# Performance work log

Hardware: AMD Instinct MI355X
Metric: run time of the kernel (lower is better)

## Reference

```python
import jax, jax.numpy as jnp
import numpy as np

N_NODES = 100000
N_EDGES = 1600000
D = 128  # conv_channels = [128, 128, 128] -> two GCNConv layers


def setup_inputs() -> dict:
    key = jax.random.key(0)
    ks = jax.random.split(key, 6)
    x = jax.random.normal(ks[0], (N_NODES, D), dtype=jnp.float32)
    edge_index = jax.random.randint(ks[1], (2, N_EDGES), 0, N_NODES, dtype=jnp.int32)
    s = 1.0 / np.sqrt(D)
    W1 = jax.random.uniform(ks[2], (D, D), jnp.float32, -s, s)
    b1 = jnp.zeros((D,), jnp.float32)
    W2 = jax.random.uniform(ks[3], (D, D), jnp.float32, -s, s)
    b2 = jnp.zeros((D,), jnp.float32)
    return {"x": x, "edge_index": edge_index, "W1": W1, "b1": b1, "W2": W2, "b2": b2}


def _gcn_layer(x, W, b, src, dst, norm, n_nodes):
    h = x @ W                       # [N, out]
    msg = h[src] * norm[:, None]    # gather + scale, [E', out]
    agg = jax.ops.segment_sum(msg, dst, num_segments=n_nodes)
    return agg + b


def reference(x, edge_index, W1, b1, W2, b2):
    n = x.shape[0]
    # add_self_loops: append (i, i) for every node
    loop = jnp.arange(n, dtype=edge_index.dtype)
    src = jnp.concatenate([edge_index[0], loop])
    dst = jnp.concatenate([edge_index[1], loop])
    # symmetric GCN normalization: deg over target nodes (unit edge weights)
    deg = jax.ops.segment_sum(jnp.ones_like(src, dtype=x.dtype), dst, num_segments=n)
    dis = jnp.where(deg > 0, jax.lax.rsqrt(deg), 0.0)
    norm = dis[src] * dis[dst]      # [E']

    h = _gcn_layer(x, W1, b1, src, dst, norm, n)
    h = jax.nn.elu(h)
    # dropout p=0.3 is identity in eval mode
    h = _gcn_layer(h, W2, b2, src, dst, norm, n)
    h = jax.nn.elu(h)
    return h
```

## Files before the change

### kernel.cpp

```cpp
#include <hip/hip_runtime.h>
#include <math.h>

#define NN 100000
#define NE 1600000
#define NT (NE + NN)
#define DD 128
#define NB 500
#define BR 200
#define BCAP 4096
#define NCH 2048
#define NBK 782
#define NBG 1563
#define PW 68
#define BMAGIC 21474837u

typedef unsigned int uint;
typedef unsigned short ushort;
typedef __attribute__((ext_vector_type(8))) short bf16x8;
typedef __attribute__((ext_vector_type(4))) float f32x4;

__device__ __forceinline__ uint bfr(float f){
  uint u = __float_as_uint(f);
  return (u + 0x7FFFu + ((u >> 16) & 1u)) >> 16;
}
__device__ __forceinline__ uint pk2(float a, float b){
  return (bfr(a) & 0xFFFFu) | (bfr(b) << 16);
}
__device__ __forceinline__ bf16x8 asbf(uint4 u){
  union { uint4 u; bf16x8 b; } c; c.u = u; return c.b;
}

__global__ __launch_bounds__(256) void k_pre1(const float* __restrict__ W1f, const float* __restrict__ W2f,
    uint* __restrict__ Wt1, uint* __restrict__ Wt2,
    const int* __restrict__ ei, int* __restrict__ gcnt, uint* __restrict__ bedge){
  __shared__ uint   ent[NCH];
  __shared__ ushort bbs[NCH];
  __shared__ int    hist[NB];
  __shared__ int    fl[NB];
  __shared__ int    gb[NB];
  int t = threadIdx.x;
  if (blockIdx.x < 2){
    const float* W = blockIdx.x ? W2f : W1f;
    uint* Wt = blockIdx.x ? Wt2 : Wt1;
    int n = t >> 1, k0 = (t & 1) * 64;
    for (int kk = 0; kk < 64; kk += 2){
      float v0 = W[(size_t)(k0+kk  )*DD + n];
      float v1 = W[(size_t)(k0+kk+1)*DD + n];
      Wt[(size_t)n*64 + ((k0+kk)>>1)] = pk2(v0, v1);
    }
    return;
  }
  int bid = blockIdx.x - 2;
  int base = bid * NCH;
  int nv = NE - base; if (nv > NCH) nv = NCH;
  for (int b = t; b < NB; b += 256){ hist[b] = 0; fl[b] = 0; }
  __syncthreads();
  for (int j = t; j < nv; j += 256){
    int i = base + j;
    uint s = (uint)ei[i];
    uint d = (uint)ei[NE + i];
    uint b = __umulhi(d, BMAGIC);
    uint dl = d - b*BR;
    ent[j] = s | (dl << 17);
    bbs[j] = (ushort)b;
    atomicAdd(&hist[b], 1);
  }
  __syncthreads();
  for (int b = t; b < NB; b += 256){
    int h = hist[b];
    gb[b] = h ? atomicAdd(&gcnt[b*16], h) : 0;
  }
  __syncthreads();
  for (int j = t; j < nv; j += 256){
    uint b = bbs[j];
    int q = atomicAdd(&fl[b], 1);
    bedge[(size_t)b*BCAP + gb[b] + q] = ent[j];
  }
}

__global__ __launch_bounds__(256) void k_pre2(const int* __restrict__ gcnt, int* __restrict__ bbase,
    const uint* __restrict__ bedge, int* __restrict__ deg, float* __restrict__ dis){
  __shared__ int sm[256];
  int t = threadIdx.x;
  if (blockIdx.x == 0){
    int i0 = 2*t, i1 = 2*t + 1;
    int v0 = (i0 < NB) ? (gcnt[i0*16] + BR) : 0;
    int v1 = (i1 < NB) ? (gcnt[i1*16] + BR) : 0;
    int p = v0 + v1;
    sm[t] = p;
    __syncthreads();
    for (int off = 1; off < 256; off <<= 1){
      int a = (t >= off) ? sm[t-off] : 0;
      __syncthreads();
      sm[t] += a;
      __syncthreads();
    }
    int excl = sm[t] - p;
    if (i0 < NB) bbase[i0] = excl;
    if (i1 < NB) bbase[i1] = excl + v0;
    return;
  }
  int b = blockIdx.x - 1;
  int* cl = sm;
  if (t < BR) cl[t] = 0;
  __syncthreads();
  int cnt = gcnt[b*16];
  for (int e = t; e < cnt; e += 256){
    atomicAdd(&cl[bedge[(size_t)b*BCAP + e] >> 17], 1);
  }
  __syncthreads();
  if (t < BR){
    int n = b*BR + t;
    int dg = cl[t];
    deg[n] = dg;
    dis[n] = rsqrtf((float)(dg + 1));
  }
}

template<int IN_BF16>
__device__ __forceinline__ void gemm_body(uint* __restrict__ Ws, uint* __restrict__ Xs,
    const void* __restrict__ Xv, const uint* __restrict__ Wt,
    const float* __restrict__ dis, uint* __restrict__ Y, int row0){
  int t = threadIdx.x;
  #pragma unroll
  for (int it = 0; it < 8; ++it){
    int f = it*256 + t;
    uint4 v = ((const uint4*)Wt)[f];
    int row = f >> 4, c4 = f & 15;
    *(uint4*)&Ws[row*PW + c4*4] = v;
  }
  if (!IN_BF16){
    const float* X = (const float*)Xv;
    #pragma unroll
    for (int it = 0; it < 8; ++it){
      int f = it*256 + t;
      int row = f >> 5, c4 = f & 31;
      int gr = row0 + row;
      float4 v = (gr < NN) ? ((const float4*)X)[(size_t)gr*32 + c4]
                           : make_float4(0.f,0.f,0.f,0.f);
      uint2 p; p.x = pk2(v.x, v.y); p.y = pk2(v.z, v.w);
      *(uint2*)&Xs[row*PW + c4*2] = p;
    }
  } else {
    const uint* X = (const uint*)Xv;
    #pragma unroll
    for (int it = 0; it < 4; ++it){
      int f = it*256 + t;
      int row = f >> 4, c4 = f & 15;
      int gr = row0 + row;
      uint4 v = (gr < NN) ? ((const uint4*)X)[(size_t)gr*16 + c4]
                          : make_uint4(0,0,0,0);
      *(uint4*)&Xs[row*PW + c4*4] = v;
    }
  }
  __syncthreads();

  int wv = t >> 6, l = t & 63;
  int g = l >> 4, li = l & 15;
  int rb = wv*16 + li;
  int r  = row0 + rb;
  f32x4 acc[8];
  #pragma unroll
  for (int i = 0; i < 8; ++i) acc[i] = (f32x4){0.f,0.f,0.f,0.f};

  #pragma unroll
  for (int ks = 0; ks < 4; ++ks){
    int c = (ks*4 + g)*4;
    bf16x8 bfrag = asbf(*(const uint4*)&Xs[rb*PW + c]);
    #pragma unroll
    for (int nt = 0; nt < 8; ++nt){
      bf16x8 afrag = asbf(*(const uint4*)&Ws[(nt*16 + li)*PW + c]);
      acc[nt] = __builtin_amdgcn_mfma_f32_16x16x32_bf16(afrag, bfrag, acc[nt], 0, 0, 0);
    }
  }
  if (r < NN){
    float dr = dis[r];
    #pragma unroll
    for (int nt = 0; nt < 8; ++nt){
      uint2 o;
      o.x = pk2(acc[nt][0]*dr, acc[nt][1]*dr);
      o.y = pk2(acc[nt][2]*dr, acc[nt][3]*dr);
      *(uint2*)&Y[(size_t)r*64 + nt*8 + g*2] = o;
    }
  }
}

__global__ __launch_bounds__(256, 3) void k_bg(const int* __restrict__ gcnt,
    const int* __restrict__ bbase, const uint* __restrict__ bedge,
    const int* __restrict__ deg, const float* __restrict__ dis,
    int* __restrict__ rowptr, uint* __restrict__ es,
    const float* __restrict__ X, const uint* __restrict__ Wt1, uint* __restrict__ H){
  __shared__ uint smem[192*PW];
  int t = threadIdx.x;
  if (blockIdx.x >= NB){
    gemm_body<0>(smem, smem + 128*PW, X, Wt1, dis, H, (blockIdx.x - NB)*64);
    return;
  }
  int b = blockIdx.x;
  int base = bbase[b];
  int* cl = (int*)smem;
  int* fl = cl + BR;
  int* pf = cl + 2*BR;
  if (t < BR){ cl[t] = deg[b*BR + t]; fl[t] = 0; }
  __syncthreads();
  int v = (t < BR) ? (cl[t] + 1) : 0;
  pf[t] = v;
  __syncthreads();
  for (int off = 1; off < 256; off <<= 1){
    int a = (t >= off) ? pf[t-off] : 0;
    __syncthreads();
    pf[t] += a;
    __syncthreads();
  }
  if (t < BR){
    int n  = b*BR + t;
    int p0 = base + pf[t] - v;
    rowptr[n] = p0;
    es[p0 + cl[t]] = (uint)n;
  }
  if (b == NB-1 && t == 0) rowptr[NN] = NT;
  __syncthreads();
  int cnt = gcnt[b*16];
  for (int e = t; e < cnt; e += 256){
    uint u = bedge[(size_t)b*BCAP + e];
    int  dloc = u >> 17;
    int  q  = atomicAdd(&fl[dloc], 1);
    int  p0 = base + pf[dloc] - (cl[dloc] + 1);
    es[p0 + q] = u & 0x1FFFFu;
  }
}

__global__ __launch_bounds__(256, 3) void k_gemm2(const uint* __restrict__ X,
    const uint* __restrict__ Wt, const float* __restrict__ dis, uint* __restrict__ Y){
  __shared__ uint smem[192*PW];
  gemm_body<1>(smem, smem + 128*PW, X, Wt, dis, Y, blockIdx.x*64);
}

template<int OUT_BF16>
__global__ __launch_bounds__(256) void k_agg(const uint* __restrict__ H,
    const int* __restrict__ rowptr, const float* __restrict__ dis,
    const uint* __restrict__ es, const float* __restrict__ bias,
    void* __restrict__ outv){
  int wid  = threadIdx.x >> 6;
  int lane = threadIdx.x & 63;
  int n = blockIdx.x*4 + wid;
  int e0 = rowptr[n];
  int e1 = rowptr[n+1];
  float a0 = 0.f, a1 = 0.f, a2 = 0.f, a3 = 0.f;
  int e = e0;

#define ASTEP(k,A,B) { uint s##k = es[e+k]; \
    uint h##k = H[(size_t)s##k*64 + lane]; \
    A += __uint_as_float(h##k << 16); \
    B += __uint_as_float(h##k & 0xFFFF0000u); }

  for (; e + 16 <= e1; e += 16){
    ASTEP( 0,a0,a1) ASTEP( 1,a2,a3) ASTEP( 2,a0,a1) ASTEP( 3,a2,a3)
    ASTEP( 4,a0,a1) ASTEP( 5,a2,a3) ASTEP( 6,a0,a1) ASTEP( 7,a2,a3)
    ASTEP( 8,a0,a1) ASTEP( 9,a2,a3) ASTEP(10,a0,a1) ASTEP(11,a2,a3)
    ASTEP(12,a0,a1) ASTEP(13,a2,a3) ASTEP(14,a0,a1) ASTEP(15,a2,a3)
  }
  for (; e + 4 <= e1; e += 4){
    ASTEP(0,a0,a1) ASTEP(1,a2,a3) ASTEP(2,a0,a1) ASTEP(3,a2,a3)
  }
  for (; e < e1; ++e){
    ASTEP(0,a0,a1)
  }
#undef ASTEP

  float dn = dis[n];
  float2 b = *(const float2*)&bias[lane*2];
  float v0 = fmaf(dn, a0 + a2, b.x);
  float v1 = fmaf(dn, a1 + a3, b.y);
  v0 = (v0 > 0.f) ? v0 : expm1f(v0);
  v1 = (v1 > 0.f) ? v1 : expm1f(v1);
  if (OUT_BF16){
    ((uint*)outv)[(size_t)n*64 + lane] = pk2(v0, v1);
  } else {
    float2 o; o.x = v0; o.y = v1;
    *(float2*)&((float*)outv)[(size_t)n*DD + lane*2] = o;
  }
}


extern "C" void kernel_launch(void* const* d_in, const int* in_sizes, int n_in,
                              void* d_out, int out_size, void* d_ws, size_t ws_size,
                              hipStream_t stream){
  const float* x  = (const float*)d_in[0];
  const int*   ei = (const int*)d_in[1];
  const float* W1 = (const float*)d_in[2];
  const float* b1 = (const float*)d_in[3];
  const float* W2 = (const float*)d_in[4];
  const float* b2 = (const float*)d_in[5];

  int*   ws_i   = (int*)d_ws;
  int*   gcnt   = ws_i + 0;
  int*   bbase  = ws_i + 8000;
  float* dis    = (float*)(ws_i + 8576);
  int*   rowptr = ws_i + 108608;
  int*   deg    = ws_i + 208704;
  uint*  Wt1    = (uint*)(ws_i + 308736);
  uint*  Wt2    = (uint*)(ws_i + 316928);
  uint*  es     = (uint*)(ws_i + 325120);
  uint*  bedge  = (uint*)(ws_i + 2025152);
  uint*  out1   = (uint*)(ws_i + 2025152);
  uint*  H      = (uint*)(ws_i + 8425152);
  uint*  H2     = H;

  hipMemsetAsync(gcnt, 0, 8000*sizeof(int), stream);

  k_pre1<<<NBK + 2, 256, 0, stream>>>(W1, W2, Wt1, Wt2, ei, gcnt, bedge);
  k_pre2<<<NB + 1,  256, 0, stream>>>(gcnt, bbase, bedge, deg, dis);
  k_bg  <<<NB + NBG,256, 0, stream>>>(gcnt, bbase, bedge, deg, dis, rowptr, es, x, Wt1, H);
  k_agg<1><<<25000, 256, 0, stream>>>(H, rowptr, dis, es, b1, out1);
  k_gemm2 <<<NBG,   256, 0, stream>>>(out1, Wt2, dis, H2);
  k_agg<0><<<25000, 256, 0, stream>>>(H2, rowptr, dis, es, b2, d_out);
}
```

Measured before the change: 233.7 us.

## Pack source-norm weights into edge list and overlap GEMM1 with bucketing

Removes the dis[r] row scaling from the GEMMs. Instead, each CSR edge entry now carries bf16(dis[src]) in its top 15 bits, and the aggregation kernel applies that weight with an FMA. Because GEMM1 no longer depends on the degree, it can run in the same launch as the edge bucketing pass. The hipMemset is replaced by a small init kernel and the CSR build becomes its own kernel. The cost is a bf16-rounded per-edge weight and an extra dis gather during CSR construction; the 15-bit field also relies on dis being positive and below 2.

Measured after the change: 243.8 us. 4.3% more time.

```diff
diff --git a/kernel.cpp b/kernel.cpp
--- a/kernel.cpp
+++ b/kernel.cpp
@@ -30,28 +30,105 @@
   union { uint4 u; bf16x8 b; } c; c.u = u; return c.b;
 }
 
-__global__ __launch_bounds__(256) void k_pre1(const float* __restrict__ W1f, const float* __restrict__ W2f,
-    uint* __restrict__ Wt1, uint* __restrict__ Wt2,
-    const int* __restrict__ ei, int* __restrict__ gcnt, uint* __restrict__ bedge){
-  __shared__ uint   ent[NCH];
-  __shared__ ushort bbs[NCH];
-  __shared__ int    hist[NB];
-  __shared__ int    fl[NB];
-  __shared__ int    gb[NB];
+__global__ __launch_bounds__(256) void k_init(const float* __restrict__ W1f, const float* __restrict__ W2f,
+    uint* __restrict__ Wt1, uint* __restrict__ Wt2, int* __restrict__ gcnt){
   int t = threadIdx.x;
-  if (blockIdx.x < 2){
-    const float* W = blockIdx.x ? W2f : W1f;
-    uint* Wt = blockIdx.x ? Wt2 : Wt1;
-    int n = t >> 1, k0 = (t & 1) * 64;
-    for (int kk = 0; kk < 64; kk += 2){
-      float v0 = W[(size_t)(k0+kk  )*DD + n];
-      float v1 = W[(size_t)(k0+kk+1)*DD + n];
-      Wt[(size_t)n*64 + ((k0+kk)>>1)] = pk2(v0, v1);
-    }
+  if (blockIdx.x == 2){
+    for (int i = t; i < 8000; i += 256) gcnt[i] = 0;
     return;
   }
-  int bid = blockIdx.x - 2;
-  int base = bid * NCH;
+  const float* W = blockIdx.x ? W2f : W1f;
+  uint* Wt = blockIdx.x ? Wt2 : Wt1;
+  int n = t >> 1, k0 = (t & 1) * 64;
+  for (int kk = 0; kk < 64; kk += 2){
+    float v0 = W[(size_t)(k0+kk  )*DD + n];
+    float v1 = W[(size_t)(k0+kk+1)*DD + n];
+    Wt[(size_t)n*64 + ((k0+kk)>>1)] = pk2(v0, v1);
+  }
+}
+
+template<int IN_BF16>
+__device__ __forceinline__ void gemm_body(uint* __restrict__ Ws, uint* __restrict__ Xs,
+    const void* __restrict__ Xv, const uint* __restrict__ Wt,
+    uint* __restrict__ Y, int row0){
+  int t = threadIdx.x;
+  #pragma unroll
+  for (int it = 0; it < 8; ++it){
+    int f = it*256 + t;
+    uint4 v = ((const uint4*)Wt)[f];
+    int row = f >> 4, c4 = f & 15;
+    *(uint4*)&Ws[row*PW + c4*4] = v;
+  }
+  if (!IN_BF16){
+    const float* X = (const float*)Xv;
+    #pragma unroll
+    for (int it = 0; it < 8; ++it){
+      int f = it*256 + t;
+      int row = f >> 5, c4 = f & 31;
+      int gr = row0 + row;
+      float4 v = (gr < NN) ? ((const float4*)X)[(size_t)gr*32 + c4]
+                           : make_float4(0.f,0.f,0.f,0.f);
+      uint2 p; p.x = pk2(v.x, v.y); p.y = pk2(v.z, v.w);
+      *(uint2*)&Xs[row*PW + c4*2] = p;
+    }
+  } else {
+    const uint* X = (const uint*)Xv;
+    #pragma unroll
+    for (int it = 0; it < 4; ++it){
+      int f = it*256 + t;
+      int row = f >> 4, c4 = f & 15;
+      int gr = row0 + row;
+      uint4 v = (gr < NN) ? ((const uint4*)X)[(size_t)gr*16 + c4]
+                          : make_uint4(0,0,0,0);
+      *(uint4*)&Xs[row*PW + c4*4] = v;
+    }
+  }
+  __syncthreads();
+
+  int wv = t >> 6, l = t & 63;
+  int g = l >> 4, li = l & 15;
+  int rb = wv*16 + li;
+  int r  = row0 + rb;
+  f32x4 acc[8];
+  #pragma unroll
+  for (int i = 0; i < 8; ++i) acc[i] = (f32x4){0.f,0.f,0.f,0.f};
+
+  #pragma unroll
+  for (int ks = 0; ks < 4; ++ks){
+    int c = (ks*4 + g)*4;
+    bf16x8 bfrag = asbf(*(const uint4*)&Xs[rb*PW + c]);
+    #pragma unroll
+    for (int nt = 0; nt < 8; ++nt){
+      bf16x8 afrag = asbf(*(const uint4*)&Ws[(nt*16 + li)*PW + c]);
+      acc[nt] = __builtin_amdgcn_mfma_f32_16x16x32_bf16(afrag, bfrag, acc[nt], 0, 0, 0);
+    }
+  }
+  if (r < NN){
+    #pragma unroll
+    for (int nt = 0; nt < 8; ++nt){
+      uint2 o;
+      o.x = pk2(acc[nt][0], acc[nt][1]);
+      o.y = pk2(acc[nt][2], acc[nt][3]);
+      *(uint2*)&Y[(size_t)r*64 + nt*8 + g*2] = o;
+    }
+  }
+}
+
+__global__ __launch_bounds__(256, 3) void k_A(const int* __restrict__ ei,
+    int* __restrict__ gcnt, uint* __restrict__ bedge,
+    const float* __restrict__ X, const uint* __restrict__ Wt1, uint* __restrict__ H){
+  __shared__ uint smem[192*PW];
+  int t = threadIdx.x;
+  if (blockIdx.x >= NBK){
+    gemm_body<0>(smem, smem + 128*PW, X, Wt1, H, (blockIdx.x - NBK)*64);
+    return;
+  }
+  uint*   ent  = smem;
+  ushort* bbs  = (ushort*)(smem + NCH);
+  int*    hist = (int*)(smem + NCH + NCH/2);
+  int*    fl   = hist + NB;
+  int*    gb   = fl + NB;
+  int base = blockIdx.x * NCH;
   int nv = NE - base; if (nv > NCH) nv = NCH;
   for (int b = t; b < NB; b += 256){ hist[b] = 0; fl[b] = 0; }
   __syncthreads();
@@ -78,7 +155,7 @@
   }
 }
 
-__global__ __launch_bounds__(256) void k_pre2(const int* __restrict__ gcnt, int* __restrict__ bbase,
+__global__ __launch_bounds__(256) void k_B(const int* __restrict__ gcnt, int* __restrict__ bbase,
     const uint* __restrict__ bedge, int* __restrict__ deg, float* __restrict__ dis){
   __shared__ int sm[256];
   int t = threadIdx.x;
@@ -117,90 +194,15 @@
   }
 }
 
-template<int IN_BF16>
-__device__ __forceinline__ void gemm_body(uint* __restrict__ Ws, uint* __restrict__ Xs,
-    const void* __restrict__ Xv, const uint* __restrict__ Wt,
-    const float* __restrict__ dis, uint* __restrict__ Y, int row0){
-  int t = threadIdx.x;
-  #pragma unroll
-  for (int it = 0; it < 8; ++it){
-    int f = it*256 + t;
-    uint4 v = ((const uint4*)Wt)[f];
-    int row = f >> 4, c4 = f & 15;
-    *(uint4*)&Ws[row*PW + c4*4] = v;
-  }
-  if (!IN_BF16){
-    const float* X = (const float*)Xv;
-    #pragma unroll
-    for (int it = 0; it < 8; ++it){
-      int f = it*256 + t;
-      int row = f >> 5, c4 = f & 31;
-      int gr = row0 + row;
-      float4 v = (gr < NN) ? ((const float4*)X)[(size_t)gr*32 + c4]
-                           : make_float4(0.f,0.f,0.f,0.f);
-      uint2 p; p.x = pk2(v.x, v.y); p.y = pk2(v.z, v.w);
-      *(uint2*)&Xs[row*PW + c4*2] = p;
-    }
-  } else {
-    const uint* X = (const uint*)Xv;
-    #pragma unroll
-    for (int it = 0; it < 4; ++it){
-      int f = it*256 + t;
-      int row = f >> 4, c4 = f & 15;
-      int gr = row0 + row;
-      uint4 v = (gr < NN) ? ((const uint4*)X)[(size_t)gr*16 + c4]
-                          : make_uint4(0,0,0,0);
-      *(uint4*)&Xs[row*PW + c4*4] = v;
-    }
-  }
-  __syncthreads();
-
-  int wv = t >> 6, l = t & 63;
-  int g = l >> 4, li = l & 15;
-  int rb = wv*16 + li;
-  int r  = row0 + rb;
-  f32x4 acc[8];
-  #pragma unroll
-  for (int i = 0; i < 8; ++i) acc[i] = (f32x4){0.f,0.f,0.f,0.f};
-
-  #pragma unroll
-  for (int ks = 0; ks < 4; ++ks){
-    int c = (ks*4 + g)*4;
-    bf16x8 bfrag = asbf(*(const uint4*)&Xs[rb*PW + c]);
-    #pragma unroll
-    for (int nt = 0; nt < 8; ++nt){
-      bf16x8 afrag = asbf(*(const uint4*)&Ws[(nt*16 + li)*PW + c]);
-      acc[nt] = __builtin_amdgcn_mfma_f32_16x16x32_bf16(afrag, bfrag, acc[nt], 0, 0, 0);
-    }
-  }
-  if (r < NN){
-    float dr = dis[r];
-    #pragma unroll
-    for (int nt = 0; nt < 8; ++nt){
-      uint2 o;
-      o.x = pk2(acc[nt][0]*dr, acc[nt][1]*dr);
-      o.y = pk2(acc[nt][2]*dr, acc[nt][3]*dr);
-      *(uint2*)&Y[(size_t)r*64 + nt*8 + g*2] = o;
-    }
-  }
-}
-
-__global__ __launch_bounds__(256, 3) void k_bg(const int* __restrict__ gcnt,
+__global__ __launch_bounds__(256) void k_C(const int* __restrict__ gcnt,
     const int* __restrict__ bbase, const uint* __restrict__ bedge,
     const int* __restrict__ deg, const float* __restrict__ dis,
-    int* __restrict__ rowptr, uint* __restrict__ es,
-    const float* __restrict__ X, const uint* __restrict__ Wt1, uint* __restrict__ H){
-  __shared__ uint smem[192*PW];
-  int t = threadIdx.x;
-  if (blockIdx.x >= NB){
-    gemm_body<0>(smem, smem + 128*PW, X, Wt1, dis, H, (blockIdx.x - NB)*64);
-    return;
-  }
-  int b = blockIdx.x;
+    int* __restrict__ rowptr, uint* __restrict__ es){
+  __shared__ int cl[BR];
+  __shared__ int fl[BR];
+  __shared__ int pf[256];
+  int b = blockIdx.x, t = threadIdx.x;
   int base = bbase[b];
-  int* cl = (int*)smem;
-  int* fl = cl + BR;
-  int* pf = cl + 2*BR;
   if (t < BR){ cl[t] = deg[b*BR + t]; fl[t] = 0; }
   __syncthreads();
   int v = (t < BR) ? (cl[t] + 1) : 0;
@@ -216,24 +218,25 @@
     int n  = b*BR + t;
     int p0 = base + pf[t] - v;
     rowptr[n] = p0;
-    es[p0 + cl[t]] = (uint)n;
+    es[p0 + cl[t]] = (uint)n | ((bfr(dis[n]) & 0x7FFFu) << 17);
   }
   if (b == NB-1 && t == 0) rowptr[NN] = NT;
   __syncthreads();
   int cnt = gcnt[b*16];
   for (int e = t; e < cnt; e += 256){
     uint u = bedge[(size_t)b*BCAP + e];
+    uint s = u & 0x1FFFFu;
     int  dloc = u >> 17;
     int  q  = atomicAdd(&fl[dloc], 1);
     int  p0 = base + pf[dloc] - (cl[dloc] + 1);
-    es[p0 + q] = u & 0x1FFFFu;
+    es[p0 + q] = s | ((bfr(dis[s]) & 0x7FFFu) << 17);
   }
 }
 
 __global__ __launch_bounds__(256, 3) void k_gemm2(const uint* __restrict__ X,
-    const uint* __restrict__ Wt, const float* __restrict__ dis, uint* __restrict__ Y){
+    const uint* __restrict__ Wt, uint* __restrict__ Y){
   __shared__ uint smem[192*PW];
-  gemm_body<1>(smem, smem + 128*PW, X, Wt, dis, Y, blockIdx.x*64);
+  gemm_body<1>(smem, smem + 128*PW, X, Wt, Y, blockIdx.x*64);
 }
 
 template<int OUT_BF16>
@@ -249,10 +252,11 @@
   float a0 = 0.f, a1 = 0.f, a2 = 0.f, a3 = 0.f;
   int e = e0;
 
-#define ASTEP(k,A,B) { uint s##k = es[e+k]; \
-    uint h##k = H[(size_t)s##k*64 + lane]; \
-    A += __uint_as_float(h##k << 16); \
-    B += __uint_as_float(h##k & 0xFFFF0000u); }
+#define ASTEP(k,A,B) { uint p##k = es[e+k]; \
+    uint h##k = H[(size_t)(p##k & 0x1FFFFu)*64 + lane]; \
+    float w##k = __uint_as_float((p##k >> 17) << 16); \
+    A = fmaf(w##k, __uint_as_float(h##k << 16), A); \
+    B = fmaf(w##k, __uint_as_float(h##k & 0xFFFF0000u), B); }
 
   for (; e + 16 <= e1; e += 16){
     ASTEP( 0,a0,a1) ASTEP( 1,a2,a3) ASTEP( 2,a0,a1) ASTEP( 3,a2,a3)
@@ -307,12 +311,11 @@
   uint*  H      = (uint*)(ws_i + 8425152);
   uint*  H2     = H;
 
-  hipMemsetAsync(gcnt, 0, 8000*sizeof(int), stream);
-
-  k_pre1<<<NBK + 2, 256, 0, stream>>>(W1, W2, Wt1, Wt2, ei, gcnt, bedge);
-  k_pre2<<<NB + 1,  256, 0, stream>>>(gcnt, bbase, bedge, deg, dis);
-  k_bg  <<<NB + NBG,256, 0, stream>>>(gcnt, bbase, bedge, deg, dis, rowptr, es, x, Wt1, H);
+  k_init<<<3, 256, 0, stream>>>(W1, W2, Wt1, Wt2, gcnt);
+  k_A   <<<NBK + NBG, 256, 0, stream>>>(ei, gcnt, bedge, x, Wt1, H);
+  k_B   <<<NB + 1, 256, 0, stream>>>(gcnt, bbase, bedge, deg, dis);
+  k_C   <<<NB, 256, 0, stream>>>(gcnt, bbase, bedge, deg, dis, rowptr, es);
   k_agg<1><<<25000, 256, 0, stream>>>(H, rowptr, dis, es, b1, out1);
-  k_gemm2 <<<NBG,   256, 0, stream>>>(out1, Wt2, dis, H2);
+  k_gemm2 <<<NBG, 256, 0, stream>>>(out1, Wt2, H2);
   k_agg<0><<<25000, 256, 0, stream>>>(H2, rowptr, dis, es, b2, d_out);
 }
```

## Merge CSR preprocessing kernels into one cooperative kernel with grid syncs

Applied to the files above, without the earlier changes.

Replaces the memset plus three preprocessing kernel launches with a single cooperative kernel of 782 blocks that zeroes counters, bins edges, computes degrees and builds the CSR, separated by grid-wide syncs. The first GEMM becomes its own kernel instead of running alongside the CSR build. This removes launch gaps and the separate memset. In exchange it adds grid.sync overhead, and it loses the overlap between the GEMM and the CSR build. It also requires all 782 blocks to be co-resident.

Result: slower. 649.9 us (+178.1%).

```diff
diff --git a/kernel.cpp b/kernel.cpp
--- a/kernel.cpp
+++ b/kernel.cpp
@@ -1,5 +1,8 @@
 #include <hip/hip_runtime.h>
+#include <hip/hip_cooperative_groups.h>
 #include <math.h>
+
+namespace cg = cooperative_groups;
 
 #define NN 100000
 #define NE 1600000
@@ -30,59 +33,69 @@
   union { uint4 u; bf16x8 b; } c; c.u = u; return c.b;
 }
 
-__global__ __launch_bounds__(256) void k_pre1(const float* __restrict__ W1f, const float* __restrict__ W2f,
+__global__ __launch_bounds__(256) void k_pre(const float* __restrict__ W1f, const float* __restrict__ W2f,
     uint* __restrict__ Wt1, uint* __restrict__ Wt2,
-    const int* __restrict__ ei, int* __restrict__ gcnt, uint* __restrict__ bedge){
-  __shared__ uint   ent[NCH];
-  __shared__ ushort bbs[NCH];
-  __shared__ int    hist[NB];
-  __shared__ int    fl[NB];
-  __shared__ int    gb[NB];
+    const int* __restrict__ ei, int* __restrict__ gcnt, uint* __restrict__ bedge,
+    int* __restrict__ bbase, int* __restrict__ deg, float* __restrict__ dis,
+    int* __restrict__ rowptr, uint* __restrict__ es){
+  __shared__ uint smem[4608];
+  cg::grid_group grid = cg::this_grid();
   int t = threadIdx.x;
-  if (blockIdx.x < 2){
-    const float* W = blockIdx.x ? W2f : W1f;
-    uint* Wt = blockIdx.x ? Wt2 : Wt1;
+  int blk = blockIdx.x;
+
+  if (blk < 2){
+    const float* W = blk ? W2f : W1f;
+    uint* Wt = blk ? Wt2 : Wt1;
     int n = t >> 1, k0 = (t & 1) * 64;
     for (int kk = 0; kk < 64; kk += 2){
       float v0 = W[(size_t)(k0+kk  )*DD + n];
       float v1 = W[(size_t)(k0+kk+1)*DD + n];
       Wt[(size_t)n*64 + ((k0+kk)>>1)] = pk2(v0, v1);
     }
-    return;
-  }
-  int bid = blockIdx.x - 2;
-  int base = bid * NCH;
-  int nv = NE - base; if (nv > NCH) nv = NCH;
-  for (int b = t; b < NB; b += 256){ hist[b] = 0; fl[b] = 0; }
-  __syncthreads();
-  for (int j = t; j < nv; j += 256){
-    int i = base + j;
-    uint s = (uint)ei[i];
-    uint d = (uint)ei[NE + i];
-    uint b = __umulhi(d, BMAGIC);
-    uint dl = d - b*BR;
-    ent[j] = s | (dl << 17);
-    bbs[j] = (ushort)b;
-    atomicAdd(&hist[b], 1);
-  }
-  __syncthreads();
-  for (int b = t; b < NB; b += 256){
-    int h = hist[b];
-    gb[b] = h ? atomicAdd(&gcnt[b*16], h) : 0;
-  }
-  __syncthreads();
-  for (int j = t; j < nv; j += 256){
-    uint b = bbs[j];
-    int q = atomicAdd(&fl[b], 1);
-    bedge[(size_t)b*BCAP + gb[b] + q] = ent[j];
-  }
-}
-
-__global__ __launch_bounds__(256) void k_pre2(const int* __restrict__ gcnt, int* __restrict__ bbase,
-    const uint* __restrict__ bedge, int* __restrict__ deg, float* __restrict__ dis){
-  __shared__ int sm[256];
-  int t = threadIdx.x;
-  if (blockIdx.x == 0){
+  } else if (blk < 34){
+    int i = (blk - 2)*256 + t;
+    if (i < 8000) gcnt[i] = 0;
+  }
+  __threadfence();
+  grid.sync();
+
+  {
+    uint*   ent  = smem;
+    ushort* bbs  = (ushort*)(smem + NCH);
+    int*    hist = (int*)(smem + NCH + NCH/2);
+    int*    fl   = hist + NB;
+    int*    gb   = fl + NB;
+    int base = blk * NCH;
+    int nv = NE - base; if (nv > NCH) nv = NCH;
+    for (int b = t; b < NB; b += 256){ hist[b] = 0; fl[b] = 0; }
+    __syncthreads();
+    for (int j = t; j < nv; j += 256){
+      int i = base + j;
+      uint s = (uint)ei[i];
+      uint d = (uint)ei[NE + i];
+      uint b = __umulhi(d, BMAGIC);
+      uint dl = d - b*BR;
+      ent[j] = s | (dl << 17);
+      bbs[j] = (ushort)b;
+      atomicAdd(&hist[b], 1);
+    }
+    __syncthreads();
+    for (int b = t; b < NB; b += 256){
+      int h = hist[b];
+      gb[b] = h ? atomicAdd(&gcnt[b*16], h) : 0;
+    }
+    __syncthreads();
+    for (int j = t; j < nv; j += 256){
+      uint b = bbs[j];
+      int q = atomicAdd(&fl[b], 1);
+      bedge[(size_t)b*BCAP + gb[b] + q] = ent[j];
+    }
+  }
+  __threadfence();
+  grid.sync();
+
+  if (blk == 0){
+    int* sm = (int*)smem;
     int i0 = 2*t, i1 = 2*t + 1;
     int v0 = (i0 < NB) ? (gcnt[i0*16] + BR) : 0;
     int v1 = (i1 < NB) ? (gcnt[i1*16] + BR) : 0;
@@ -98,22 +111,59 @@
     int excl = sm[t] - p;
     if (i0 < NB) bbase[i0] = excl;
     if (i1 < NB) bbase[i1] = excl + v0;
-    return;
-  }
-  int b = blockIdx.x - 1;
-  int* cl = sm;
-  if (t < BR) cl[t] = 0;
-  __syncthreads();
-  int cnt = gcnt[b*16];
-  for (int e = t; e < cnt; e += 256){
-    atomicAdd(&cl[bedge[(size_t)b*BCAP + e] >> 17], 1);
-  }
-  __syncthreads();
-  if (t < BR){
-    int n = b*BR + t;
-    int dg = cl[t];
-    deg[n] = dg;
-    dis[n] = rsqrtf((float)(dg + 1));
+  } else if (blk <= NB){
+    int b = blk - 1;
+    int* cl = (int*)smem;
+    if (t < BR) cl[t] = 0;
+    __syncthreads();
+    int cnt = gcnt[b*16];
+    for (int e = t; e < cnt; e += 256){
+      atomicAdd(&cl[bedge[(size_t)b*BCAP + e] >> 17], 1);
+    }
+    __syncthreads();
+    if (t < BR){
+      int n = b*BR + t;
+      int dg = cl[t];
+      deg[n] = dg;
+      dis[n] = rsqrtf((float)(dg + 1));
+    }
+  }
+  __threadfence();
+  grid.sync();
+
+  if (blk < NB){
+    int b = blk;
+    int base = bbase[b];
+    int* cl = (int*)smem;
+    int* fl = cl + BR;
+    int* pf = cl + 2*BR;
+    if (t < BR){ cl[t] = deg[b*BR + t]; fl[t] = 0; }
+    __syncthreads();
+    int v = (t < BR) ? (cl[t] + 1) : 0;
+    pf[t] = v;
+    __syncthreads();
+    for (int off = 1; off < 256; off <<= 1){
+      int a = (t >= off) ? pf[t-off] : 0;
+      __syncthreads();
+      pf[t] += a;
+      __syncthreads();
+    }
+    if (t < BR){
+      int n  = b*BR + t;
+      int p0 = base + pf[t] - v;
+      rowptr[n] = p0;
+      es[p0 + cl[t]] = (uint)n;
+    }
+    if (b == NB-1 && t == 0) rowptr[NN] = NT;
+    __syncthreads();
+    int cnt = gcnt[b*16];
+    for (int e = t; e < cnt; e += 256){
+      uint u = bedge[(size_t)b*BCAP + e];
+      int  dloc = u >> 17;
+      int  q  = atomicAdd(&fl[dloc], 1);
+      int  p0 = base + pf[dloc] - (cl[dloc] + 1);
+      es[p0 + q] = u & 0x1FFFFu;
+    }
   }
 }
 
@@ -185,49 +235,10 @@
   }
 }
 
-__global__ __launch_bounds__(256, 3) void k_bg(const int* __restrict__ gcnt,
-    const int* __restrict__ bbase, const uint* __restrict__ bedge,
-    const int* __restrict__ deg, const float* __restrict__ dis,
-    int* __restrict__ rowptr, uint* __restrict__ es,
-    const float* __restrict__ X, const uint* __restrict__ Wt1, uint* __restrict__ H){
+__global__ __launch_bounds__(256, 3) void k_gemm1(const float* __restrict__ X,
+    const uint* __restrict__ Wt, const float* __restrict__ dis, uint* __restrict__ Y){
   __shared__ uint smem[192*PW];
-  int t = threadIdx.x;
-  if (blockIdx.x >= NB){
-    gemm_body<0>(smem, smem + 128*PW, X, Wt1, dis, H, (blockIdx.x - NB)*64);
-    return;
-  }
-  int b = blockIdx.x;
-  int base = bbase[b];
-  int* cl = (int*)smem;
-  int* fl = cl + BR;
-  int* pf = cl + 2*BR;
-  if (t < BR){ cl[t] = deg[b*BR + t]; fl[t] = 0; }
-  __syncthreads();
-  int v = (t < BR) ? (cl[t] + 1) : 0;
-  pf[t] = v;
-  __syncthreads();
-  for (int off = 1; off < 256; off <<= 1){
-    int a = (t >= off) ? pf[t-off] : 0;
-    __syncthreads();
-    pf[t] += a;
-    __syncthreads();
-  }
-  if (t < BR){
-    int n  = b*BR + t;
-    int p0 = base + pf[t] - v;
-    rowptr[n] = p0;
-    es[p0 + cl[t]] = (uint)n;
-  }
-  if (b == NB-1 && t == 0) rowptr[NN] = NT;
-  __syncthreads();
-  int cnt = gcnt[b*16];
-  for (int e = t; e < cnt; e += 256){
-    uint u = bedge[(size_t)b*BCAP + e];
-    int  dloc = u >> 17;
-    int  q  = atomicAdd(&fl[dloc], 1);
-    int  p0 = base + pf[dloc] - (cl[dloc] + 1);
-    es[p0 + q] = u & 0x1FFFFu;
-  }
+  gemm_body<0>(smem, smem + 128*PW, X, Wt, dis, Y, blockIdx.x*64);
 }
 
 __global__ __launch_bounds__(256, 3) void k_gemm2(const uint* __restrict__ X,
@@ -307,11 +318,13 @@
   uint*  H      = (uint*)(ws_i + 8425152);
   uint*  H2     = H;
 
-  hipMemsetAsync(gcnt, 0, 8000*sizeof(int), stream);
-
-  k_pre1<<<NBK + 2, 256, 0, stream>>>(W1, W2, Wt1, Wt2, ei, gcnt, bedge);
-  k_pre2<<<NB + 1,  256, 0, stream>>>(gcnt, bbase, bedge, deg, dis);
-  k_bg  <<<NB + NBG,256, 0, stream>>>(gcnt, bbase, bedge, deg, dis, rowptr, es, x, Wt1, H);
+  void* args[] = {(void*)&W1, (void*)&W2, (void*)&Wt1, (void*)&Wt2,
+                  (void*)&ei, (void*)&gcnt, (void*)&bedge,
+                  (void*)&bbase, (void*)&deg, (void*)&dis,
+                  (void*)&rowptr, (void*)&es};
+  hipLaunchCooperativeKernel((void*)k_pre, dim3(NBK), dim3(256), args, 0, stream);
+
+  k_gemm1 <<<NBG,   256, 0, stream>>>(x, Wt1, dis, H);
   k_agg<1><<<25000, 256, 0, stream>>>(H, rowptr, dis, es, b1, out1);
   k_gemm2 <<<NBG,   256, 0, stream>>>(out1, Wt2, dis, H2);
   k_agg<0><<<25000, 256, 0, stream>>>(H2, rowptr, dis, es, b2, d_out);
```
